# Kernel tuning notes

Measured on AMD Instinct MI355X. Metric: run time of the kernel, lower is better.

## Reference

```python
import jax, jax.numpy as jnp
import numpy as np

N_EMB = 1024
N_HEAD = 16
HEAD_DIM = N_EMB // N_HEAD


def setup_inputs() -> dict:
    key = jax.random.key(0)
    k_x, k_wa, k_ba, k_wp, k_bp = jax.random.split(key, 5)
    B, S = 4, 2048
    scale = 1.0 / np.sqrt(N_EMB)
    return {
        "x": jax.random.normal(k_x, (B, S, N_EMB), dtype=jnp.float32),
        "W_attn": jax.random.normal(k_wa, (N_EMB, 3 * N_EMB), dtype=jnp.float32) * scale,
        "b_attn": jax.random.normal(k_ba, (3 * N_EMB,), dtype=jnp.float32) * 0.01,
        "W_proj": jax.random.normal(k_wp, (N_EMB, N_EMB), dtype=jnp.float32) * scale,
        "b_proj": jax.random.normal(k_bp, (N_EMB,), dtype=jnp.float32) * 0.01,
    }


def _attention(x, W_attn, b_attn, W_proj, b_proj):
    B, S, E = x.shape
    qkv = x @ W_attn + b_attn  # [B, S, 3E]
    q, k, v = jnp.split(qkv, 3, axis=-1)
    # [B, H, S, D]
    q = q.reshape(B, S, N_HEAD, HEAD_DIM).transpose(0, 2, 1, 3)
    k = k.reshape(B, S, N_HEAD, HEAD_DIM).transpose(0, 2, 1, 3)
    v = v.reshape(B, S, N_HEAD, HEAD_DIM).transpose(0, 2, 1, 3)
    scores = jnp.einsum("bhqd,bhkd->bhqk", q, k) / jnp.sqrt(jnp.asarray(HEAD_DIM, x.dtype))
    causal = jnp.tril(jnp.ones((S, S), dtype=bool))
    scores = jnp.where(causal, scores, jnp.asarray(-jnp.inf, x.dtype))
    probs = jax.nn.softmax(scores, axis=-1)
    y = jnp.einsum("bhqk,bhkd->bhqd", probs, v)  # [B, H, S, D]
    y = y.transpose(0, 2, 1, 3).reshape(B, S, E)
    return y @ W_proj + b_proj


def reference(x, W_attn, b_attn, W_proj, b_proj):
    return _attention(x, W_attn, b_attn, W_proj, b_proj)
```

## Files before the change

kernel.cpp:

```cpp
#include <hip/hip_runtime.h>
#include <hip/hip_bf16.h>

typedef __bf16 bf16x8 __attribute__((ext_vector_type(8)));
typedef __bf16 bf16x4 __attribute__((ext_vector_type(4)));
typedef float f32x4 __attribute__((ext_vector_type(4)));

#define MFMA16(a, b, c) __builtin_amdgcn_mfma_f32_16x16x32_bf16(a, b, c, 0, 0, 0)

#define BATCH 4
#define SEQ   2048
#define EMB   1024
#define NHEAD 16
#define HDIM  64
#define ROWS  (BATCH * SEQ)
#define N_QKV (3 * EMB)
#define BH_STRIDE (SEQ * HDIM)

__device__ __forceinline__ void gload_lds16(const __bf16* gp, __bf16* lp) {
  __builtin_amdgcn_global_load_lds(
      (const __attribute__((address_space(1))) void*)gp,
      (__attribute__((address_space(3))) void*)lp, 16, 0, 0);
}

__global__ void cast_f32_to_bf16_x4(const float* __restrict__ src,
                                    __bf16* __restrict__ dst, int n4) {
  int i = blockIdx.x * blockDim.x + threadIdx.x;
  if (i >= n4) return;
  float4 f = ((const float4*)src)[i];
  bf16x4 o;
  o.x = (__bf16)f.x; o.y = (__bf16)f.y; o.z = (__bf16)f.z; o.w = (__bf16)f.w;
  ((bf16x4*)dst)[i] = o;
}

__global__ void transpose_to_bf16(const float* __restrict__ src,
                                  __bf16* __restrict__ dst, int R, int C) {
  __shared__ float t[32][33];
  int c0 = blockIdx.x * 32, r0 = blockIdx.y * 32;
  int tx = threadIdx.x, ty = threadIdx.y;
#pragma unroll
  for (int i = 0; i < 32; i += 8)
    t[ty + i][tx] = src[(size_t)(r0 + ty + i) * C + c0 + tx];
  __syncthreads();
#pragma unroll
  for (int i = 0; i < 32; i += 8)
    dst[(size_t)(c0 + ty + i) * R + r0 + tx] = (__bf16)t[tx][ty + i];
}

__global__ __launch_bounds__(256) void gemm_qkv(
    const __bf16* __restrict__ A, const __bf16* __restrict__ Bt,
    const float* __restrict__ bias,
    __bf16* __restrict__ Qt, __bf16* __restrict__ Kt, __bf16* __restrict__ Vt) {
  const int K = EMB;
  __shared__ __align__(16) __bf16 sA[128 * 32];
  __shared__ __align__(16) __bf16 sB[128 * 32];
  int id = blockIdx.x;
  int lid = (id & 7) * (1536 >> 3) + (id >> 3);
  int bx = lid % 24, by = lid / 24;
  int m0 = by * 128, n0 = bx * 128;
  int tid = threadIdx.x;
  int wave = tid >> 6, lane = tid & 63;
  int wr = wave >> 1, wc = wave & 1;
  int l16 = lane & 15, quad = lane >> 4;
  int f1 = tid * 8;
  int r1 = f1 >> 5, c1 = f1 & 31;
  int f2 = f1 + 2048;
  int r2 = f2 >> 5, c2 = f2 & 31;
  f32x4 acc[4][4] = {};
  for (int k0 = 0; k0 < K; k0 += 32) {
    gload_lds16(A + (size_t)(m0 + r1) * K + k0 + c1, &sA[wave * 512]);
    gload_lds16(A + (size_t)(m0 + r2) * K + k0 + c2, &sA[2048 + wave * 512]);
    gload_lds16(Bt + (size_t)(n0 + r1) * K + k0 + c1, &sB[wave * 512]);
    gload_lds16(Bt + (size_t)(n0 + r2) * K + k0 + c2, &sB[2048 + wave * 512]);
    __syncthreads();
    bf16x8 a[4], b[4];
#pragma unroll
    for (int i = 0; i < 4; i++)
      a[i] = *(const bf16x8*)(sA + (wr * 64 + i * 16 + l16) * 32 + quad * 8);
#pragma unroll
    for (int j = 0; j < 4; j++)
      b[j] = *(const bf16x8*)(sB + (wc * 64 + j * 16 + l16) * 32 + quad * 8);
#pragma unroll
    for (int i = 0; i < 4; i++)
#pragma unroll
      for (int j = 0; j < 4; j++) acc[i][j] = MFMA16(a[i], b[j], acc[i][j]);
    __syncthreads();
  }
  const float KSC = 0.18033688011112043f;
  int sec = n0 >> 10;
#pragma unroll
  for (int i = 0; i < 4; i++) {
    int row = m0 + wr * 64 + i * 16 + quad * 4;
    int bidx = row >> 11;
    int srow = row & 2047;
#pragma unroll
    for (int j = 0; j < 4; j++) {
      int col = n0 + wc * 64 + j * 16 + l16;
      float bv = bias[col];
      int e = col & 1023;
      int h = e >> 6, d = e & 63;
      size_t base = (size_t)(bidx * NHEAD + h) * BH_STRIDE;
      if (sec == 0) {
        int idx = (srow >> 4) * 1024 + (d >> 5) * 512 + quad * 32 +
                  ((d >> 3) & 3) * 128 + (d & 7);
#pragma unroll
        for (int r = 0; r < 4; r++)
          Qt[base + idx + r * 8] = (__bf16)((acc[i][j][r] + bv) * KSC);
      } else if (sec == 1) {
        int idx = (srow >> 6) * 4096 + ((srow >> 4) & 3) * 1024 + (d >> 5) * 512 +
                  quad * 32 + ((d >> 3) & 3) * 128 + (d & 7);
#pragma unroll
        for (int r = 0; r < 4; r++)
          Kt[base + idx + r * 8] = (__bf16)(acc[i][j][r] + bv);
      } else {
        int idx = (srow >> 6) * 4096 + (d >> 4) * 1024 + ((srow >> 5) & 1) * 512 +
                  (d & 15) * 8 + (((i & 1) * 2 + (quad >> 1))) * 128 + (quad & 1) * 4;
        bf16x4 o4;
        o4.x = (__bf16)(acc[i][j][0] + bv);
        o4.y = (__bf16)(acc[i][j][1] + bv);
        o4.z = (__bf16)(acc[i][j][2] + bv);
        o4.w = (__bf16)(acc[i][j][3] + bv);
        *(bf16x4*)(Vt + base + idx) = o4;
      }
    }
  }
}

#define PS2 68
__global__ __launch_bounds__(256, 8) void attn_fwd(
    const __bf16* __restrict__ Qt, const __bf16* __restrict__ Kt,
    const __bf16* __restrict__ Vt, __bf16* __restrict__ Y) {
  __shared__ __align__(16) __bf16 pbuf[4][16 * PS2];
  int id = blockIdx.x;
  int qb = id >> 6;
  int hb = id & 63;
  int h = hb >> 2, b = hb & 3;
  int wave = threadIdx.x >> 6, lane = threadIdx.x & 63;
  int l16 = lane & 15, quad = lane >> 4;
  int quad4 = quad * 4;
  int q0 = qb * 64;
  size_t bh = (size_t)b * NHEAD + h;
  const __bf16* Qh = Qt + bh * BH_STRIDE;
  const __bf16* Kh = Kt + bh * BH_STRIDE;
  const __bf16* Vh = Vt + bh * BH_STRIDE;
  int mq = q0 + wave * 16;
  const __bf16* qbase = Qh + (size_t)(mq >> 4) * 1024 + lane * 8;
  bf16x8 qf0 = *(const bf16x8*)(qbase);
  bf16x8 qf1 = *(const bf16x8*)(qbase + 512);
  f32x4 acc[4] = {};
  float l_part = 0.f;
  const float NEG_INF = -__builtin_inff();
  __bf16* pw = pbuf[wave];
  int kt_end = q0 + 64;
  for (int kt = 0; kt < kt_end; kt += 64) {
    const __bf16* kp = Kh + (size_t)(kt >> 6) * 4096 + lane * 8;
    bool diag = (kt + 64 > mq);
    int rel = mq + l16 - kt;
#pragma unroll
    for (int t = 0; t < 4; t++) {
      bf16x8 ka = *(const bf16x8*)(kp + t * 1024);
      bf16x8 kb = *(const bf16x8*)(kp + t * 1024 + 512);
      f32x4 z = {};
      z = MFMA16(ka, qf0, z);
      z = MFMA16(kb, qf1, z);
      float p0, p1, p2, p3;
      if (diag) {
        int kl = t * 16 + quad4;
        p0 = __builtin_amdgcn_exp2f(kl + 0 > rel ? NEG_INF : z[0]);
        p1 = __builtin_amdgcn_exp2f(kl + 1 > rel ? NEG_INF : z[1]);
        p2 = __builtin_amdgcn_exp2f(kl + 2 > rel ? NEG_INF : z[2]);
        p3 = __builtin_amdgcn_exp2f(kl + 3 > rel ? NEG_INF : z[3]);
      } else {
        p0 = __builtin_amdgcn_exp2f(z[0]);
        p1 = __builtin_amdgcn_exp2f(z[1]);
        p2 = __builtin_amdgcn_exp2f(z[2]);
        p3 = __builtin_amdgcn_exp2f(z[3]);
      }
      l_part += (p0 + p1) + (p2 + p3);
      bf16x4 o4;
      o4.x = (__bf16)p0; o4.y = (__bf16)p1;
      o4.z = (__bf16)p2; o4.w = (__bf16)p3;
      *(bf16x4*)(pw + l16 * PS2 + t * 16 + quad4) = o4;
    }
    bf16x8 pf0 = *(const bf16x8*)(pw + l16 * PS2 + quad * 8);
    bf16x8 pf1 = *(const bf16x8*)(pw + l16 * PS2 + 32 + quad * 8);
    const __bf16* vp = Vh + (size_t)(kt >> 6) * 4096 + lane * 8;
#pragma unroll
    for (int jj = 0; jj < 4; jj++) {
      bf16x8 va = *(const bf16x8*)(vp + jj * 1024);
      bf16x8 vb = *(const bf16x8*)(vp + jj * 1024 + 512);
      acc[jj] = MFMA16(va, pf0, acc[jj]);
      acc[jj] = MFMA16(vb, pf1, acc[jj]);
    }
  }
  float lt = l_part;
  lt += __shfl_xor(lt, 16);
  lt += __shfl_xor(lt, 32);
  float inv = 1.f / lt;
  int gq = mq + l16;
#pragma unroll
  for (int jj = 0; jj < 4; jj++) {
    bf16x4 o4;
    o4.x = (__bf16)(acc[jj][0] * inv);
    o4.y = (__bf16)(acc[jj][1] * inv);
    o4.z = (__bf16)(acc[jj][2] * inv);
    o4.w = (__bf16)(acc[jj][3] * inv);
    *(bf16x4*)(Y + ((size_t)b * SEQ + gq) * EMB + h * HDIM + jj * 16 + quad4) = o4;
  }
}

__global__ __launch_bounds__(256) void gemm_proj(
    const __bf16* __restrict__ A, const __bf16* __restrict__ Bt,
    const float* __restrict__ bias, float* __restrict__ out) {
  const int K = EMB;
  __shared__ __align__(16) __bf16 sA[128 * 32];
  __shared__ __align__(16) __bf16 sB[128 * 32];
  int id = blockIdx.x;
  int lid = (id & 7) * (512 >> 3) + (id >> 3);
  int bx = lid & 7, by = lid >> 3;
  int m0 = by * 128, n0 = bx * 128;
  int tid = threadIdx.x;
  int wave = tid >> 6, lane = tid & 63;
  int wr = wave >> 1, wc = wave & 1;
  int l16 = lane & 15, quad = lane >> 4;
  int f1 = tid * 8;
  int r1 = f1 >> 5, c1 = f1 & 31;
  int f2 = f1 + 2048;
  int r2 = f2 >> 5, c2 = f2 & 31;
  f32x4 acc[4][4] = {};
  for (int k0 = 0; k0 < K; k0 += 32) {
    gload_lds16(A + (size_t)(m0 + r1) * K + k0 + c1, &sA[wave * 512]);
    gload_lds16(A + (size_t)(m0 + r2) * K + k0 + c2, &sA[2048 + wave * 512]);
    gload_lds16(Bt + (size_t)(n0 + r1) * K + k0 + c1, &sB[wave * 512]);
    gload_lds16(Bt + (size_t)(n0 + r2) * K + k0 + c2, &sB[2048 + wave * 512]);
    __syncthreads();
    bf16x8 a[4], b[4];
#pragma unroll
    for (int i = 0; i < 4; i++)
      a[i] = *(const bf16x8*)(sA + (wr * 64 + i * 16 + l16) * 32 + quad * 8);
#pragma unroll
    for (int j = 0; j < 4; j++)
      b[j] = *(const bf16x8*)(sB + (wc * 64 + j * 16 + l16) * 32 + quad * 8);
#pragma unroll
    for (int i = 0; i < 4; i++)
#pragma unroll
      for (int j = 0; j < 4; j++) acc[i][j] = MFMA16(a[i], b[j], acc[i][j]);
    __syncthreads();
  }
#pragma unroll
  for (int i = 0; i < 4; i++) {
    int row = m0 + wr * 64 + i * 16 + quad * 4;
#pragma unroll
    for (int j = 0; j < 4; j++) {
      int col = n0 + wc * 64 + j * 16 + l16;
      float bv = bias[col];
#pragma unroll
      for (int r = 0; r < 4; r++)
        out[(size_t)(row + r) * EMB + col] = acc[i][j][r] + bv;
    }
  }
}

extern "C" void kernel_launch(void* const* d_in, const int* in_sizes, int n_in,
                              void* d_out, int out_size, void* d_ws, size_t ws_size,
                              hipStream_t stream) {
  const float* x      = (const float*)d_in[0];
  const float* W_attn = (const float*)d_in[1];
  const float* b_attn = (const float*)d_in[2];
  const float* W_proj = (const float*)d_in[3];
  const float* b_proj = (const float*)d_in[4];
  float* out = (float*)d_out;

  char* ws = (char*)d_ws;
  size_t off = 0;
  __bf16* xb   = (__bf16*)(ws + off); off += (size_t)ROWS * EMB * 2;
  __bf16* Wa_t = (__bf16*)(ws + off); off += (size_t)N_QKV * EMB * 2;
  __bf16* Wp_t = (__bf16*)(ws + off); off += (size_t)EMB * EMB * 2;
  __bf16* Qt   = (__bf16*)(ws + off); off += (size_t)ROWS * EMB * 2;
  __bf16* Kt   = (__bf16*)(ws + off); off += (size_t)ROWS * EMB * 2;
  __bf16* Vt   = (__bf16*)(ws + off); off += (size_t)ROWS * EMB * 2;
  __bf16* Yb   = (__bf16*)(ws + off); off += (size_t)ROWS * EMB * 2;

  {
    int n4 = ROWS * EMB / 4;
    cast_f32_to_bf16_x4<<<(n4 + 255) / 256, 256, 0, stream>>>(x, xb, n4);
    dim3 blk(32, 8);
    transpose_to_bf16<<<dim3(N_QKV / 32, EMB / 32), blk, 0, stream>>>(W_attn, Wa_t, EMB, N_QKV);
    transpose_to_bf16<<<dim3(EMB / 32, EMB / 32), blk, 0, stream>>>(W_proj, Wp_t, EMB, EMB);
  }
  gemm_qkv<<<dim3(1536), 256, 0, stream>>>(xb, Wa_t, b_attn, Qt, Kt, Vt);
  attn_fwd<<<dim3(SEQ / 64 * NHEAD * BATCH), 256, 0, stream>>>(Qt, Kt, Vt, Yb);
  gemm_proj<<<dim3(512), 256, 0, stream>>>(Yb, Wp_t, b_proj, out);
}
```

Baseline: 283.0 us.

## Stage K/V tiles in LDS, process 128 queries per block, swap QKV GEMM operands

The attention kernel now handles 128 query rows per block, with each wave covering 32 rows, and stages each 64-key K/V tile in shared memory via global_load_lds. All four waves share those tiles instead of each reading K and V from global memory. Query blocks are issued in a heavy/light interleaved order to balance the causal workload. The QKV GEMM swaps its A/B operands so bias loads and output stores become vectorized along the head dimension. In exchange, occupancy drops (launch bounds 8→4), block-level syncs are added, and there are half as many attention blocks.

```diff
diff --git a/kernel.cpp b/kernel.cpp
--- a/kernel.cpp
+++ b/kernel.cpp
@@ -54,13 +54,14 @@
   __shared__ __align__(16) __bf16 sA[128 * 32];
   __shared__ __align__(16) __bf16 sB[128 * 32];
   int id = blockIdx.x;
-  int lid = (id & 7) * (1536 >> 3) + (id >> 3);
-  int bx = lid % 24, by = lid / 24;
+  int xcd = id & 7, j5 = id >> 3;
+  int by = j5 >> 3;
+  int bx = xcd * 8 + (j5 & 7);
   int m0 = by * 128, n0 = bx * 128;
   int tid = threadIdx.x;
   int wave = tid >> 6, lane = tid & 63;
   int wr = wave >> 1, wc = wave & 1;
-  int l16 = lane & 15, quad = lane >> 4;
+  int l16 = lane & 15, quad = lane >> 4, quad4 = quad * 4;
   int f1 = tid * 8;
   int r1 = f1 >> 5, c1 = f1 & 31;
   int f2 = f1 + 2048;
@@ -86,125 +87,157 @@
     __syncthreads();
   }
   const float KSC = 0.18033688011112043f;
-  int sec = n0 >> 10;
+  int sec = m0 >> 10;
 #pragma unroll
   for (int i = 0; i < 4; i++) {
-    int row = m0 + wr * 64 + i * 16 + quad * 4;
-    int bidx = row >> 11;
-    int srow = row & 2047;
+    int e0 = m0 + wr * 64 + i * 16 + quad4;
+    float4 bv4 = *(const float4*)(bias + e0);
+    int h = (e0 & 1023) >> 6, d0 = e0 & 63;
 #pragma unroll
     for (int j = 0; j < 4; j++) {
-      int col = n0 + wc * 64 + j * 16 + l16;
-      float bv = bias[col];
-      int e = col & 1023;
-      int h = e >> 6, d = e & 63;
+      int scol = n0 + wc * 64 + j * 16 + l16;
+      int bidx = scol >> 11, s = scol & 2047;
       size_t base = (size_t)(bidx * NHEAD + h) * BH_STRIDE;
+      float v0 = acc[i][j][0] + bv4.x;
+      float v1 = acc[i][j][1] + bv4.y;
+      float v2 = acc[i][j][2] + bv4.z;
+      float v3 = acc[i][j][3] + bv4.w;
       if (sec == 0) {
-        int idx = (srow >> 4) * 1024 + (d >> 5) * 512 + quad * 32 +
-                  ((d >> 3) & 3) * 128 + (d & 7);
-#pragma unroll
-        for (int r = 0; r < 4; r++)
-          Qt[base + idx + r * 8] = (__bf16)((acc[i][j][r] + bv) * KSC);
+        int idx = (s >> 4) * 1024 + (d0 >> 5) * 512 + ((d0 >> 3) & 3) * 128 +
+                  (s & 15) * 8 + (d0 & 7);
+        bf16x4 o4;
+        o4.x = (__bf16)(v0 * KSC); o4.y = (__bf16)(v1 * KSC);
+        o4.z = (__bf16)(v2 * KSC); o4.w = (__bf16)(v3 * KSC);
+        *(bf16x4*)(Qt + base + idx) = o4;
       } else if (sec == 1) {
-        int idx = (srow >> 6) * 4096 + ((srow >> 4) & 3) * 1024 + (d >> 5) * 512 +
-                  quad * 32 + ((d >> 3) & 3) * 128 + (d & 7);
-#pragma unroll
-        for (int r = 0; r < 4; r++)
-          Kt[base + idx + r * 8] = (__bf16)(acc[i][j][r] + bv);
+        int idx = (s >> 6) * 4096 + ((s >> 4) & 3) * 1024 + (d0 >> 5) * 512 +
+                  ((d0 >> 3) & 3) * 128 + (s & 15) * 8 + (d0 & 7);
+        bf16x4 o4;
+        o4.x = (__bf16)v0; o4.y = (__bf16)v1;
+        o4.z = (__bf16)v2; o4.w = (__bf16)v3;
+        *(bf16x4*)(Kt + base + idx) = o4;
       } else {
-        int idx = (srow >> 6) * 4096 + (d >> 4) * 1024 + ((srow >> 5) & 1) * 512 +
-                  (d & 15) * 8 + (((i & 1) * 2 + (quad >> 1))) * 128 + (quad & 1) * 4;
-        bf16x4 o4;
-        o4.x = (__bf16)(acc[i][j][0] + bv);
-        o4.y = (__bf16)(acc[i][j][1] + bv);
-        o4.z = (__bf16)(acc[i][j][2] + bv);
-        o4.w = (__bf16)(acc[i][j][3] + bv);
-        *(bf16x4*)(Vt + base + idx) = o4;
+        int idx = (s >> 6) * 4096 + (d0 >> 4) * 1024 + ((s >> 5) & 1) * 512 +
+                  ((s >> 3) & 3) * 128 + (s & 7) + quad4 * 8;
+        Vt[base + idx] = (__bf16)v0;
+        Vt[base + idx + 8] = (__bf16)v1;
+        Vt[base + idx + 16] = (__bf16)v2;
+        Vt[base + idx + 24] = (__bf16)v3;
       }
     }
   }
 }
 
 #define PS2 68
-__global__ __launch_bounds__(256, 8) void attn_fwd(
+__global__ __launch_bounds__(256, 4) void attn_fwd(
     const __bf16* __restrict__ Qt, const __bf16* __restrict__ Kt,
     const __bf16* __restrict__ Vt, __bf16* __restrict__ Y) {
-  __shared__ __align__(16) __bf16 pbuf[4][16 * PS2];
+  __shared__ __align__(16) __bf16 sK[4096];
+  __shared__ __align__(16) __bf16 sV[4096];
+  __shared__ __align__(16) __bf16 pbuf[4][32 * PS2];
   int id = blockIdx.x;
-  int qb = id >> 6;
+  int g = id >> 6;
+  int gg = g & 3, sel = g >> 2;
+  int qb = sel == 0 ? gg : sel == 1 ? 15 - gg : sel == 2 ? 4 + gg : 11 - gg;
   int hb = id & 63;
   int h = hb >> 2, b = hb & 3;
-  int wave = threadIdx.x >> 6, lane = threadIdx.x & 63;
-  int l16 = lane & 15, quad = lane >> 4;
-  int quad4 = quad * 4;
-  int q0 = qb * 64;
+  int tid = threadIdx.x;
+  int wave = tid >> 6, lane = tid & 63;
+  int l16 = lane & 15, quad = lane >> 4, quad4 = quad * 4;
+  int q0 = qb * 128;
   size_t bh = (size_t)b * NHEAD + h;
   const __bf16* Qh = Qt + bh * BH_STRIDE;
   const __bf16* Kh = Kt + bh * BH_STRIDE;
   const __bf16* Vh = Vt + bh * BH_STRIDE;
-  int mq = q0 + wave * 16;
+  int mq = q0 + wave * 32;
   const __bf16* qbase = Qh + (size_t)(mq >> 4) * 1024 + lane * 8;
-  bf16x8 qf0 = *(const bf16x8*)(qbase);
-  bf16x8 qf1 = *(const bf16x8*)(qbase + 512);
-  f32x4 acc[4] = {};
-  float l_part = 0.f;
+  bf16x8 qa0 = *(const bf16x8*)(qbase);
+  bf16x8 qa1 = *(const bf16x8*)(qbase + 512);
+  bf16x8 qb0 = *(const bf16x8*)(qbase + 1024);
+  bf16x8 qb1 = *(const bf16x8*)(qbase + 1536);
+  f32x4 accA[4] = {}, accB[4] = {};
+  float lA = 0.f, lB = 0.f;
   const float NEG_INF = -__builtin_inff();
-  __bf16* pw = pbuf[wave];
-  int kt_end = q0 + 64;
+  __bf16* pwA = pbuf[wave];
+  __bf16* pwB = pbuf[wave] + 16 * PS2;
+  int kt_end = q0 + 128;
   for (int kt = 0; kt < kt_end; kt += 64) {
-    const __bf16* kp = Kh + (size_t)(kt >> 6) * 4096 + lane * 8;
+    const __bf16* kg = Kh + (size_t)(kt >> 6) * 4096 + tid * 8;
+    const __bf16* vg = Vh + (size_t)(kt >> 6) * 4096 + tid * 8;
+    gload_lds16(kg, sK + tid * 8);
+    gload_lds16(kg + 2048, sK + 2048 + tid * 8);
+    gload_lds16(vg, sV + tid * 8);
+    gload_lds16(vg + 2048, sV + 2048 + tid * 8);
+    __syncthreads();
     bool diag = (kt + 64 > mq);
-    int rel = mq + l16 - kt;
+    int relA = mq + l16 - kt;
 #pragma unroll
     for (int t = 0; t < 4; t++) {
-      bf16x8 ka = *(const bf16x8*)(kp + t * 1024);
-      bf16x8 kb = *(const bf16x8*)(kp + t * 1024 + 512);
-      f32x4 z = {};
-      z = MFMA16(ka, qf0, z);
-      z = MFMA16(kb, qf1, z);
-      float p0, p1, p2, p3;
+      bf16x8 ka = *(const bf16x8*)(sK + t * 1024 + lane * 8);
+      bf16x8 kb = *(const bf16x8*)(sK + t * 1024 + 512 + lane * 8);
+      f32x4 zA = {}, zB = {};
+      zA = MFMA16(ka, qa0, zA);
+      zA = MFMA16(kb, qa1, zA);
+      zB = MFMA16(ka, qb0, zB);
+      zB = MFMA16(kb, qb1, zB);
+      int kl = t * 16 + quad4;
+      float pA[4], pB[4];
       if (diag) {
-        int kl = t * 16 + quad4;
-        p0 = __builtin_amdgcn_exp2f(kl + 0 > rel ? NEG_INF : z[0]);
-        p1 = __builtin_amdgcn_exp2f(kl + 1 > rel ? NEG_INF : z[1]);
-        p2 = __builtin_amdgcn_exp2f(kl + 2 > rel ? NEG_INF : z[2]);
-        p3 = __builtin_amdgcn_exp2f(kl + 3 > rel ? NEG_INF : z[3]);
+        int relB = relA + 16;
+#pragma unroll
+        for (int r = 0; r < 4; r++) {
+          pA[r] = __builtin_amdgcn_exp2f(kl + r > relA ? NEG_INF : zA[r]);
+          pB[r] = __builtin_amdgcn_exp2f(kl + r > relB ? NEG_INF : zB[r]);
+        }
       } else {
-        p0 = __builtin_amdgcn_exp2f(z[0]);
-        p1 = __builtin_amdgcn_exp2f(z[1]);
-        p2 = __builtin_amdgcn_exp2f(z[2]);
-        p3 = __builtin_amdgcn_exp2f(z[3]);
+#pragma unroll
+        for (int r = 0; r < 4; r++) {
+          pA[r] = __builtin_amdgcn_exp2f(zA[r]);
+          pB[r] = __builtin_amdgcn_exp2f(zB[r]);
+        }
       }
-      l_part += (p0 + p1) + (p2 + p3);
-      bf16x4 o4;
-      o4.x = (__bf16)p0; o4.y = (__bf16)p1;
-      o4.z = (__bf16)p2; o4.w = (__bf16)p3;
-      *(bf16x4*)(pw + l16 * PS2 + t * 16 + quad4) = o4;
+      lA += (pA[0] + pA[1]) + (pA[2] + pA[3]);
+      lB += (pB[0] + pB[1]) + (pB[2] + pB[3]);
+      bf16x4 oA, oB;
+      oA.x = (__bf16)pA[0]; oA.y = (__bf16)pA[1];
+      oA.z = (__bf16)pA[2]; oA.w = (__bf16)pA[3];
+      oB.x = (__bf16)pB[0]; oB.y = (__bf16)pB[1];
+      oB.z = (__bf16)pB[2]; oB.w = (__bf16)pB[3];
+      *(bf16x4*)(pwA + l16 * PS2 + kl) = oA;
+      *(bf16x4*)(pwB + l16 * PS2 + kl) = oB;
     }
-    bf16x8 pf0 = *(const bf16x8*)(pw + l16 * PS2 + quad * 8);
-    bf16x8 pf1 = *(const bf16x8*)(pw + l16 * PS2 + 32 + quad * 8);
-    const __bf16* vp = Vh + (size_t)(kt >> 6) * 4096 + lane * 8;
+    bf16x8 pA0 = *(const bf16x8*)(pwA + l16 * PS2 + quad * 8);
+    bf16x8 pA1 = *(const bf16x8*)(pwA + l16 * PS2 + 32 + quad * 8);
+    bf16x8 pB0 = *(const bf16x8*)(pwB + l16 * PS2 + quad * 8);
+    bf16x8 pB1 = *(const bf16x8*)(pwB + l16 * PS2 + 32 + quad * 8);
 #pragma unroll
     for (int jj = 0; jj < 4; jj++) {
-      bf16x8 va = *(const bf16x8*)(vp + jj * 1024);
-      bf16x8 vb = *(const bf16x8*)(vp + jj * 1024 + 512);
-      acc[jj] = MFMA16(va, pf0, acc[jj]);
-      acc[jj] = MFMA16(vb, pf1, acc[jj]);
+      bf16x8 va = *(const bf16x8*)(sV + jj * 1024 + lane * 8);
+      bf16x8 vb = *(const bf16x8*)(sV + jj * 1024 + 512 + lane * 8);
+      accA[jj] = MFMA16(va, pA0, accA[jj]);
+      accA[jj] = MFMA16(vb, pA1, accA[jj]);
+      accB[jj] = MFMA16(va, pB0, accB[jj]);
+      accB[jj] = MFMA16(vb, pB1, accB[jj]);
     }
-  }
-  float lt = l_part;
-  lt += __shfl_xor(lt, 16);
-  lt += __shfl_xor(lt, 32);
-  float inv = 1.f / lt;
-  int gq = mq + l16;
+    __syncthreads();
+  }
+  lA += __shfl_xor(lA, 16); lA += __shfl_xor(lA, 32);
+  lB += __shfl_xor(lB, 16); lB += __shfl_xor(lB, 32);
+  float invA = 1.f / lA, invB = 1.f / lB;
+  int gqA = mq + l16, gqB = mq + 16 + l16;
 #pragma unroll
   for (int jj = 0; jj < 4; jj++) {
-    bf16x4 o4;
-    o4.x = (__bf16)(acc[jj][0] * inv);
-    o4.y = (__bf16)(acc[jj][1] * inv);
-    o4.z = (__bf16)(acc[jj][2] * inv);
-    o4.w = (__bf16)(acc[jj][3] * inv);
-    *(bf16x4*)(Y + ((size_t)b * SEQ + gq) * EMB + h * HDIM + jj * 16 + quad4) = o4;
+    bf16x4 oA, oB;
+    oA.x = (__bf16)(accA[jj][0] * invA);
+    oA.y = (__bf16)(accA[jj][1] * invA);
+    oA.z = (__bf16)(accA[jj][2] * invA);
+    oA.w = (__bf16)(accA[jj][3] * invA);
+    oB.x = (__bf16)(accB[jj][0] * invB);
+    oB.y = (__bf16)(accB[jj][1] * invB);
+    oB.z = (__bf16)(accB[jj][2] * invB);
+    oB.w = (__bf16)(accB[jj][3] * invB);
+    *(bf16x4*)(Y + ((size_t)b * SEQ + gqA) * EMB + h * HDIM + jj * 16 + quad4) = oA;
+    *(bf16x4*)(Y + ((size_t)b * SEQ + gqB) * EMB + h * HDIM + jj * 16 + quad4) = oB;
   }
 }
 
@@ -287,7 +320,7 @@
     transpose_to_bf16<<<dim3(N_QKV / 32, EMB / 32), blk, 0, stream>>>(W_attn, Wa_t, EMB, N_QKV);
     transpose_to_bf16<<<dim3(EMB / 32, EMB / 32), blk, 0, stream>>>(W_proj, Wp_t, EMB, EMB);
   }
-  gemm_qkv<<<dim3(1536), 256, 0, stream>>>(xb, Wa_t, b_attn, Qt, Kt, Vt);
-  attn_fwd<<<dim3(SEQ / 64 * NHEAD * BATCH), 256, 0, stream>>>(Qt, Kt, Vt, Yb);
+  gemm_qkv<<<dim3(1536), 256, 0, stream>>>(Wa_t, xb, b_attn, Qt, Kt, Vt);
+  attn_fwd<<<dim3((SEQ / 128) * NHEAD * BATCH), 256, 0, stream>>>(Qt, Kt, Vt, Yb);
   gemm_proj<<<dim3(512), 256, 0, stream>>>(Yb, Wp_t, b_proj, out);
 }
```

Measured after the change: 258.9 us. 1.09x faster.
